# Optimization experiments

Measured on AMD Instinct MI355X. Metric: run time of the kernel, lower is better.

The kernel has to match this reference:

```python
import jax, jax.numpy as jnp
import numpy as np


def setup_inputs() -> dict:
    key = jax.random.key(0)
    k1, k2, k3, k4 = jax.random.split(key, 4)
    B, S, E, H = 8, 2048, 1024, 64
    x = jax.random.normal(k1, (B, S, E), dtype=jnp.float32)
    scale = 1.0 / np.sqrt(E)
    Wq = jax.random.normal(k2, (E, H), dtype=jnp.float32) * scale
    Wk = jax.random.normal(k3, (E, H), dtype=jnp.float32) * scale
    Wv = jax.random.normal(k4, (E, H), dtype=jnp.float32) * scale
    return {"x": x, "Wq": Wq, "Wk": Wk, "Wv": Wv}


def reference(x, Wq, Wk, Wv):
    # x: [B, S, E]; Wq/Wk/Wv: [E, H]
    B, S, E = x.shape
    H = Wq.shape[1]
    q = x @ Wq  # [B, S, H]
    k = x @ Wk
    v = x @ Wv
    inv_sqrt_h = 1.0 / jnp.sqrt(jnp.asarray(H, dtype=x.dtype))
    att = jnp.einsum("bqh,bkh->bqk", q, k) * inv_sqrt_h  # [B, S, S]
    causal = jnp.tril(jnp.ones((S, S), dtype=bool))
    att = jnp.where(causal, att, jnp.asarray(-jnp.inf, dtype=att.dtype))
    att = jax.nn.softmax(att, axis=-1)
    # dropout p=0.0 (eval) -> identity
    return jnp.einsum("bqk,bkh->bqh", att, v)  # [B, S, H]
```

## Files before the change

kernel.cpp:

```cpp
#include <hip/hip_runtime.h>
#include <math.h>

typedef __attribute__((ext_vector_type(8))) short bf16x8;
typedef __attribute__((ext_vector_type(16))) float fx16;

#define SEQ 2048
#define HD 64

__device__ __forceinline__ unsigned f2bf_bits(float f){
  unsigned u = __float_as_uint(f);
  return (u + 0x7fffu + ((u >> 16) & 1u)) >> 16;
}
__device__ __forceinline__ unsigned cvt_pk_bf16(float a, float b){
  unsigned r;
  asm("v_cvt_pk_bf16_f32 %0, %1, %2" : "=v"(r) : "v"(a), "v"(b));
  return r;
}
__device__ __forceinline__ float lo16f(unsigned u){ return __uint_as_float(u << 16); }
__device__ __forceinline__ float hi16f(unsigned u){ return __uint_as_float(u & 0xffff0000u); }
union U8 { bf16x8 v; short s[8]; unsigned u[4]; };

__device__ __forceinline__ fx16 mfma_bf16(bf16x8 a, bf16x8 b, fx16 c){
  return __builtin_amdgcn_mfma_f32_32x32x16_bf16(a, b, c, 0, 0, 0);
}
__device__ __forceinline__ fx16 fzero(){
  fx16 z;
#pragma unroll
  for (int i = 0; i < 16; ++i) z[i] = 0.f;
  return z;
}

__global__ __launch_bounds__(256) void wconv_kernel(
    const float* __restrict__ Wq, const float* __restrict__ Wk, const float* __restrict__ Wv,
    short* __restrict__ wsB)
{
  int gid = blockIdx.x * 4 + (threadIdx.x >> 6);
  int lane = threadIdx.x & 63;
  int l31 = lane & 31, h = lane >> 5;
  int half = gid & 1;
  int rem = gid >> 1;
  int t = rem % 6;
  int stage = rem / 6;
  int n = t * 32 + l31;
  int mat = n >> 6, col = n & 63;
  const float* W = (mat == 0) ? Wq : (mat == 1) ? Wk : Wv;
  int kbase = stage * 16 + h * 8;
  U8 o;
#pragma unroll
  for (int i = 0; i < 8; ++i) {
    float f = W[(size_t)(kbase + i) * 64 + col];
    unsigned hb = f2bf_bits(f);
    if (half == 0) o.s[i] = (short)hb;
    else {
      float hf = __uint_as_float(hb << 16);
      o.s[i] = (short)f2bf_bits(f - hf);
    }
  }
  *(bf16x8*)(wsB + (size_t)gid * 512 + lane * 8) = o.v;
}

__global__ __launch_bounds__(256) void proj_kernel(
    const float* __restrict__ x, const short* __restrict__ wsB,
    short* __restrict__ qh, short* __restrict__ ql,
    short* __restrict__ kh, short* __restrict__ kl,
    short* __restrict__ vth, short* __restrict__ vtl)
{
  __shared__ float Rx[6 * 16 * 64];
  __shared__ float Vb[32 * 68];

  const int tid = threadIdx.x;
  const int lane = tid & 63, w = tid >> 6;
  const int l31 = lane & 31, h = lane >> 5;
  const int nsel = w & 1;
  const int ksel = w >> 1;
  const int row0 = blockIdx.x * 32;
  const size_t xbase = (size_t)(row0 + l31) * 1024;

  fx16 acc[3];
#pragma unroll
  for (int t = 0; t < 3; ++t) acc[t] = fzero();

#pragma unroll 4
  for (int s = 0; s < 32; ++s) {
    const int stage = ksel * 32 + s;
    const int k = stage * 16 + h * 8;
    float4 fa = *(const float4*)(x + xbase + k);
    float4 fb = *(const float4*)(x + xbase + k + 4);
    U8 ah, al;
    ah.u[0] = cvt_pk_bf16(fa.x, fa.y);
    ah.u[1] = cvt_pk_bf16(fa.z, fa.w);
    ah.u[2] = cvt_pk_bf16(fb.x, fb.y);
    ah.u[3] = cvt_pk_bf16(fb.z, fb.w);
    al.u[0] = cvt_pk_bf16(fa.x - lo16f(ah.u[0]), fa.y - hi16f(ah.u[0]));
    al.u[1] = cvt_pk_bf16(fa.z - lo16f(ah.u[1]), fa.w - hi16f(ah.u[1]));
    al.u[2] = cvt_pk_bf16(fb.x - lo16f(ah.u[2]), fb.y - hi16f(ah.u[2]));
    al.u[3] = cvt_pk_bf16(fb.z - lo16f(ah.u[3]), fb.w - hi16f(ah.u[3]));
#pragma unroll
    for (int tt = 0; tt < 3; ++tt) {
      const int tg = nsel * 3 + tt;
      const size_t g2 = ((size_t)stage * 6 + tg) * 2;
      bf16x8 Bh = *(const bf16x8*)(wsB + g2 * 512 + lane * 8);
      bf16x8 Bl = *(const bf16x8*)(wsB + g2 * 512 + 512 + lane * 8);
      acc[tt] = mfma_bf16(al.v, Bh, acc[tt]);
      acc[tt] = mfma_bf16(ah.v, Bl, acc[tt]);
      acc[tt] = mfma_bf16(ah.v, Bh, acc[tt]);
    }
  }

  if (ksel == 1) {
#pragma unroll
    for (int t = 0; t < 3; ++t) {
      const int tg = nsel * 3 + t;
#pragma unroll
      for (int r = 0; r < 16; ++r)
        Rx[tg * 1024 + r * 64 + lane] = acc[t][r];
    }
  }
  __syncthreads();
  if (ksel == 0) {
#pragma unroll
    for (int t = 0; t < 3; ++t) {
      const int tg = nsel * 3 + t;
      const int mat = tg >> 1;
      const int colb = (tg & 1) * 32 + l31;
      if (mat < 2) {
        short* dh = (mat == 0) ? qh : kh;
        short* dl = (mat == 0) ? ql : kl;
#pragma unroll
        for (int r = 0; r < 16; ++r) {
          float f = acc[t][r] + Rx[tg * 1024 + r * 64 + lane];
          int rowg = row0 + (r & 3) + 8 * (r >> 2) + 4 * h;
          unsigned hb = f2bf_bits(f);
          float hf = __uint_as_float(hb << 16);
          unsigned lb = f2bf_bits(f - hf);
          dh[(size_t)rowg * 64 + colb] = (short)hb;
          dl[(size_t)rowg * 64 + colb] = (short)lb;
        }
      } else {
#pragma unroll
        for (int r = 0; r < 16; ++r) {
          float f = acc[t][r] + Rx[tg * 1024 + r * 64 + lane];
          int srel = (r & 3) + 8 * (r >> 2) + 4 * h;
          Vb[srel * 68 + (tg - 4) * 32 + l31] = f;
        }
      }
    }
  }
  __syncthreads();
  {
    int d = tid >> 2, s8 = (tid & 3) * 8;
    int bb = row0 >> 11, s0 = row0 & 2047;
    U8 hv, lv;
#pragma unroll
    for (int ss = 0; ss < 8; ++ss) {
      float f = Vb[(s8 + ss) * 68 + d];
      unsigned hb = f2bf_bits(f);
      float hf = __uint_as_float(hb << 16);
      hv.s[ss] = (short)hb;
      lv.s[ss] = (short)f2bf_bits(f - hf);
    }
    size_t o = (size_t)(bb * 64 + d) * 2048 + s0 + s8;
    *(bf16x8*)(vth + o) = hv.v;
    *(bf16x8*)(vtl + o) = lv.v;
  }
}

__global__ __launch_bounds__(64) void attn_kernel(
    const short* __restrict__ qh, const short* __restrict__ ql,
    const short* __restrict__ kh, const short* __restrict__ kl,
    const short* __restrict__ vth, const short* __restrict__ vtl,
    float* __restrict__ segO, float* __restrict__ segL, float* __restrict__ segM)
{
  const int bid = blockIdx.x;
  const int b = bid & 7;
  const int r = bid >> 3;
  int g = 0;
  while (r >= 4 * (g + 1) * (g + 2)) ++g;
  const int rr = r - 4 * g * (g + 1);
  const int qt = g * 8 + rr / (g + 1);
  const int sg = rr % (g + 1);
  const int nk = qt + 1;
  const int nsg = g + 1;
  const int bs = nk / nsg, rem = nk % nsg;
  const int nsteps = bs + (sg < rem ? 1 : 0);
  const int kt0 = sg * bs + (sg < rem ? sg : rem);

  const int lane = threadIdx.x;
  const int l31 = lane & 31, h = lane >> 5;
  const int qabs = qt * 32 + l31;

  bf16x8 qf0[4], qf1[4];
  {
    size_t qrow = ((size_t)b * 2048 + qabs) * 64;
#pragma unroll
    for (int ds = 0; ds < 4; ++ds) {
      qf0[ds] = *(const bf16x8*)(qh + qrow + ds * 16 + 8 * h);
      qf1[ds] = *(const bf16x8*)(ql + qrow + ds * 16 + 8 * h);
    }
  }

  fx16 acc0 = fzero(), acc1 = fzero();
  float Mrun = -3e38f, lrun = 0.f;

  bf16x8 kah[4], kal[4];
  {
    const size_t koff = ((size_t)b * 2048 + (size_t)kt0 * 32 + l31) * 64 + 8 * h;
#pragma unroll
    for (int ds = 0; ds < 4; ++ds) {
      kah[ds] = *(const bf16x8*)(kh + koff + ds * 16);
      kal[ds] = *(const bf16x8*)(kl + koff + ds * 16);
    }
  }

  for (int it = 0; it < nsteps; ++it) {
    const int kt = kt0 + it;
    bf16x8 vfh[2][2], vfl[2][2];
#pragma unroll
    for (int kp = 0; kp < 2; ++kp)
#pragma unroll
      for (int md = 0; md < 2; ++md) {
        const size_t vrow = (size_t)(b * 64 + md * 32 + l31) * 2048 + kt * 32 + kp * 16 + 8 * h;
        vfh[kp][md] = *(const bf16x8*)(vth + vrow);
        vfl[kp][md] = *(const bf16x8*)(vtl + vrow);
      }
    const int kn = (it + 1 < nsteps) ? kt + 1 : kt;
    bf16x8 knh[4], knl[4];
    {
      const size_t koff = ((size_t)b * 2048 + (size_t)kn * 32 + l31) * 64 + 8 * h;
#pragma unroll
      for (int ds = 0; ds < 4; ++ds) {
        knh[ds] = *(const bf16x8*)(kh + koff + ds * 16);
        knl[ds] = *(const bf16x8*)(kl + koff + ds * 16);
      }
    }

    fx16 stA = fzero(), stB = fzero();
    __builtin_amdgcn_s_setprio(1);
#pragma unroll
    for (int ds = 0; ds < 4; ++ds) {
      stA = mfma_bf16(kah[ds], qf0[ds], stA);
      stB = mfma_bf16(kal[ds], qf0[ds], stB);
      stB = mfma_bf16(kah[ds], qf1[ds], stB);
    }
    __builtin_amdgcn_s_setprio(0);

    float sv[16];
    const bool diag = (kt == qt);
#pragma unroll
    for (int r2 = 0; r2 < 16; ++r2) {
      float s = (stA[r2] + stB[r2]) * 0.125f;
      if (diag) {
        int ka = kt * 32 + (r2 & 3) + 8 * (r2 >> 2) + 4 * h;
        if (ka > qabs) s = -3e38f;
      }
      sv[r2] = s;
    }
    float tm = sv[0];
#pragma unroll
    for (int r2 = 1; r2 < 16; ++r2) tm = fmaxf(tm, sv[r2]);
    tm = fmaxf(tm, __shfl_xor(tm, 32, 64));
    float Mnew = fmaxf(Mrun, tm);
    float alpha = __expf(Mrun - Mnew);
    Mrun = Mnew;
    float psum = 0.f;
#pragma unroll
    for (int r2 = 0; r2 < 16; ++r2) { sv[r2] = __expf(sv[r2] - Mnew); psum += sv[r2]; }
    psum += __shfl_xor(psum, 32, 64);
    lrun = lrun * alpha + psum;
#pragma unroll
    for (int r2 = 0; r2 < 16; ++r2) { acc0[r2] *= alpha; acc1[r2] *= alpha; }

    unsigned chv[8], clv[8];
#pragma unroll
    for (int q2 = 0; q2 < 8; ++q2) {
      unsigned c = cvt_pk_bf16(sv[2 * q2], sv[2 * q2 + 1]);
      chv[q2] = c;
      clv[q2] = cvt_pk_bf16(sv[2 * q2] - lo16f(c), sv[2 * q2 + 1] - hi16f(c));
    }
#pragma unroll
    for (int kp = 0; kp < 2; ++kp) {
      U8 ph, pl;
      {
        unsigned c0 = chv[4 * kp], c1 = chv[4 * kp + 1], c2 = chv[4 * kp + 2], c3 = chv[4 * kp + 3];
        unsigned x0 = (unsigned)__shfl_xor((int)c0, 32, 64);
        unsigned x1 = (unsigned)__shfl_xor((int)c1, 32, 64);
        unsigned x2 = (unsigned)__shfl_xor((int)c2, 32, 64);
        unsigned x3 = (unsigned)__shfl_xor((int)c3, 32, 64);
        ph.u[0] = h ? x2 : c0;  ph.u[1] = h ? x3 : c1;
        ph.u[2] = h ? c2 : x0;  ph.u[3] = h ? c3 : x1;
        c0 = clv[4 * kp]; c1 = clv[4 * kp + 1]; c2 = clv[4 * kp + 2]; c3 = clv[4 * kp + 3];
        x0 = (unsigned)__shfl_xor((int)c0, 32, 64);
        x1 = (unsigned)__shfl_xor((int)c1, 32, 64);
        x2 = (unsigned)__shfl_xor((int)c2, 32, 64);
        x3 = (unsigned)__shfl_xor((int)c3, 32, 64);
        pl.u[0] = h ? x2 : c0;  pl.u[1] = h ? x3 : c1;
        pl.u[2] = h ? c2 : x0;  pl.u[3] = h ? c3 : x1;
      }
      __builtin_amdgcn_s_setprio(1);
      acc0 = mfma_bf16(vfl[kp][0], ph.v, acc0);
      acc0 = mfma_bf16(vfh[kp][0], pl.v, acc0);
      acc0 = mfma_bf16(vfh[kp][0], ph.v, acc0);
      acc1 = mfma_bf16(vfl[kp][1], ph.v, acc1);
      acc1 = mfma_bf16(vfh[kp][1], pl.v, acc1);
      acc1 = mfma_bf16(vfh[kp][1], ph.v, acc1);
      __builtin_amdgcn_s_setprio(0);
    }
#pragma unroll
    for (int ds = 0; ds < 4; ++ds) { kah[ds] = knh[ds]; kal[ds] = knl[ds]; }
  }

  float* o = segO + (size_t)bid * 2048;
#pragma unroll
  for (int md = 0; md < 2; ++md) {
#pragma unroll
    for (int r2 = 0; r2 < 16; ++r2) {
      int d = md * 32 + (r2 & 3) + 8 * (r2 >> 2) + 4 * h;
      float val = md ? acc1[r2] : acc0[r2];
      o[d * 32 + l31] = val;
    }
  }
  if (h == 0) {
    segL[(size_t)bid * 32 + l31] = lrun;
    segM[(size_t)bid * 32 + l31] = Mrun;
  }
}

__global__ __launch_bounds__(256) void combine_kernel(
    const float* __restrict__ segO, const float* __restrict__ segL,
    const float* __restrict__ segM, float* __restrict__ out)
{
  __shared__ float Sc[8][32];
  __shared__ float Linv[32];
  __shared__ float Ot[64 * 40];

  const int bq = blockIdx.x;
  const int b = bq >> 6, qt = bq & 63;
  const int g = qt >> 3, nsg = g + 1;
  const int base = 4 * g * (g + 1) + (qt & 7) * nsg;
  const int tid = threadIdx.x;

  if (tid < 32) {
    float M = -3e38f;
    for (int s = 0; s < nsg; ++s)
      M = fmaxf(M, segM[(size_t)((base + s) * 8 + b) * 32 + tid]);
    float L = 0.f;
    for (int s = 0; s < nsg; ++s) {
      float e = __expf(segM[(size_t)((base + s) * 8 + b) * 32 + tid] - M);
      Sc[s][tid] = e;
      L += e * segL[(size_t)((base + s) * 8 + b) * 32 + tid];
    }
    Linv[tid] = 1.f / L;
  }
  __syncthreads();
  {
#pragma unroll
    for (int i = tid; i < 512; i += 256) {
      int d = i >> 3, q4 = (i & 7) * 4;
      float4 acc = {0.f, 0.f, 0.f, 0.f};
      for (int s = 0; s < nsg; ++s) {
        float4 v = *(const float4*)(segO + (size_t)((base + s) * 8 + b) * 2048 + d * 32 + q4);
        acc.x += Sc[s][q4 + 0] * v.x;
        acc.y += Sc[s][q4 + 1] * v.y;
        acc.z += Sc[s][q4 + 2] * v.z;
        acc.w += Sc[s][q4 + 3] * v.w;
      }
      *(float4*)&Ot[d * 40 + q4] = acc;
    }
  }
  __syncthreads();
  {
    const int q = tid >> 3, dc = (tid & 7) * 8;
    const float inv = Linv[q];
    float* dst = out + ((size_t)b * 2048 + qt * 32 + q) * 64 + dc;
#pragma unroll
    for (int i = 0; i < 2; ++i) {
      float4 o;
      o.x = Ot[(dc + 4 * i + 0) * 40 + q] * inv;
      o.y = Ot[(dc + 4 * i + 1) * 40 + q] * inv;
      o.z = Ot[(dc + 4 * i + 2) * 40 + q] * inv;
      o.w = Ot[(dc + 4 * i + 3) * 40 + q] * inv;
      *(float4*)(dst + 4 * i) = o;
    }
  }
}

extern "C" void kernel_launch(void* const* d_in, const int* in_sizes, int n_in,
                              void* d_out, int out_size, void* d_ws, size_t ws_size,
                              hipStream_t stream) {
  const float* x  = (const float*)d_in[0];
  const float* Wq = (const float*)d_in[1];
  const float* Wk = (const float*)d_in[2];
  const float* Wv = (const float*)d_in[3];

  char* wsb = (char*)d_ws;
  short* wsB = (short*)(wsb + 0);
  short* qh  = (short*)(wsb + 786432);
  short* ql  = (short*)(wsb + 2883584);
  short* kh  = (short*)(wsb + 4980736);
  short* kl  = (short*)(wsb + 7077888);
  short* vth = (short*)(wsb + 9175040);
  short* vtl = (short*)(wsb + 11272192);
  float* segO = (float*)(wsb + 13369344);
  float* segL = (float*)(wsb + 32243712);
  float* segM = (float*)(wsb + 32538624);

  wconv_kernel<<<192, 256, 0, stream>>>(Wq, Wk, Wv, wsB);
  proj_kernel<<<512, 256, 0, stream>>>(x, wsB, qh, ql, kh, kl, vth, vtl);
  attn_kernel<<<2304, 64, 0, stream>>>(qh, ql, kh, kl, vth, vtl, segO, segL, segM);
  combine_kernel<<<512, 256, 0, stream>>>(segO, segL, segM, (float*)d_out);
}
```

Measured before the change: 97.79 us.

## Split projection K-reduction over 8 waves and use fixed 5-tile attention segments

The projection kernel now uses 512 threads, splitting the K dimension four ways instead of two, with a two-level shared-memory reduction of partial accumulators. The attention split-K scheme changes from group-based segments to fixed segments of at most five key tiles, which raises the block count to 3536 and evens out per-block work. The software prefetch of the next K tile is removed and K is loaded at the start of each step. The aim is more parallelism and better load balance, at the cost of extra reduction syncs, more segment partials for the combine kernel to read, and less latency hiding in attention.

```diff
diff --git a/kernel.cpp b/kernel.cpp
--- a/kernel.cpp
+++ b/kernel.cpp
@@ -59,20 +59,20 @@
   *(bf16x8*)(wsB + (size_t)gid * 512 + lane * 8) = o.v;
 }
 
-__global__ __launch_bounds__(256) void proj_kernel(
+__global__ __launch_bounds__(512) void proj_kernel(
     const float* __restrict__ x, const short* __restrict__ wsB,
     short* __restrict__ qh, short* __restrict__ ql,
     short* __restrict__ kh, short* __restrict__ kl,
     short* __restrict__ vth, short* __restrict__ vtl)
 {
-  __shared__ float Rx[6 * 16 * 64];
+  __shared__ float Rx[4][3 * 16 * 64];
   __shared__ float Vb[32 * 68];
 
   const int tid = threadIdx.x;
   const int lane = tid & 63, w = tid >> 6;
   const int l31 = lane & 31, h = lane >> 5;
+  const int ksel = w >> 1;
   const int nsel = w & 1;
-  const int ksel = w >> 1;
   const int row0 = blockIdx.x * 32;
   const size_t xbase = (size_t)(row0 + l31) * 1024;
 
@@ -81,8 +81,8 @@
   for (int t = 0; t < 3; ++t) acc[t] = fzero();
 
 #pragma unroll 4
-  for (int s = 0; s < 32; ++s) {
-    const int stage = ksel * 32 + s;
+  for (int s = 0; s < 16; ++s) {
+    const int stage = ksel * 16 + s;
     const int k = stage * 16 + h * 8;
     float4 fa = *(const float4*)(x + xbase + k);
     float4 fb = *(const float4*)(x + xbase + k + 4);
@@ -107,14 +107,30 @@
     }
   }
 
-  if (ksel == 1) {
-#pragma unroll
-    for (int t = 0; t < 3; ++t) {
-      const int tg = nsel * 3 + t;
+  if (ksel == 1 || ksel == 3) {
+    const int ws_ = (ksel == 1) ? nsel : 2 + nsel;
+#pragma unroll
+    for (int t = 0; t < 3; ++t)
 #pragma unroll
       for (int r = 0; r < 16; ++r)
-        Rx[tg * 1024 + r * 64 + lane] = acc[t][r];
-    }
+        Rx[ws_][t * 1024 + r * 64 + lane] = acc[t][r];
+  }
+  __syncthreads();
+  if (ksel == 0 || ksel == 2) {
+    const int rs_ = (ksel == 0) ? nsel : 2 + nsel;
+#pragma unroll
+    for (int t = 0; t < 3; ++t)
+#pragma unroll
+      for (int r = 0; r < 16; ++r)
+        acc[t][r] += Rx[rs_][t * 1024 + r * 64 + lane];
+  }
+  __syncthreads();
+  if (ksel == 2) {
+#pragma unroll
+    for (int t = 0; t < 3; ++t)
+#pragma unroll
+      for (int r = 0; r < 16; ++r)
+        Rx[nsel][t * 1024 + r * 64 + lane] = acc[t][r];
   }
   __syncthreads();
   if (ksel == 0) {
@@ -123,12 +139,15 @@
       const int tg = nsel * 3 + t;
       const int mat = tg >> 1;
       const int colb = (tg & 1) * 32 + l31;
+#pragma unroll
+      for (int r = 0; r < 16; ++r)
+        acc[t][r] += Rx[nsel][t * 1024 + r * 64 + lane];
       if (mat < 2) {
         short* dh = (mat == 0) ? qh : kh;
         short* dl = (mat == 0) ? ql : kl;
 #pragma unroll
         for (int r = 0; r < 16; ++r) {
-          float f = acc[t][r] + Rx[tg * 1024 + r * 64 + lane];
+          float f = acc[t][r];
           int rowg = row0 + (r & 3) + 8 * (r >> 2) + 4 * h;
           unsigned hb = f2bf_bits(f);
           float hf = __uint_as_float(hb << 16);
@@ -139,7 +158,7 @@
       } else {
 #pragma unroll
         for (int r = 0; r < 16; ++r) {
-          float f = acc[t][r] + Rx[tg * 1024 + r * 64 + lane];
+          float f = acc[t][r];
           int srel = (r & 3) + 8 * (r >> 2) + 4 * h;
           Vb[srel * 68 + (tg - 4) * 32 + l31] = f;
         }
@@ -147,7 +166,7 @@
     }
   }
   __syncthreads();
-  {
+  if (tid < 256) {
     int d = tid >> 2, s8 = (tid & 3) * 8;
     int bb = row0 >> 11, s0 = row0 & 2047;
     U8 hv, lv;
@@ -173,17 +192,13 @@
 {
   const int bid = blockIdx.x;
   const int b = bid & 7;
-  const int r = bid >> 3;
-  int g = 0;
-  while (r >= 4 * (g + 1) * (g + 2)) ++g;
-  const int rr = r - 4 * g * (g + 1);
-  const int qt = g * 8 + rr / (g + 1);
-  const int sg = rr % (g + 1);
+  int r = bid >> 3;
+  int qt = 0, acc = 0;
+  while (r >= acc + ((qt + 5) / 5)) { acc += (qt + 5) / 5; ++qt; }
+  const int sg = r - acc;
   const int nk = qt + 1;
-  const int nsg = g + 1;
-  const int bs = nk / nsg, rem = nk % nsg;
-  const int nsteps = bs + (sg < rem ? 1 : 0);
-  const int kt0 = sg * bs + (sg < rem ? sg : rem);
+  const int kt0 = sg * 5;
+  int nsteps = nk - kt0; if (nsteps > 5) nsteps = 5;
 
   const int lane = threadIdx.x;
   const int l31 = lane & 31, h = lane >> 5;
@@ -202,18 +217,17 @@
   fx16 acc0 = fzero(), acc1 = fzero();
   float Mrun = -3e38f, lrun = 0.f;
 
-  bf16x8 kah[4], kal[4];
-  {
-    const size_t koff = ((size_t)b * 2048 + (size_t)kt0 * 32 + l31) * 64 + 8 * h;
-#pragma unroll
-    for (int ds = 0; ds < 4; ++ds) {
-      kah[ds] = *(const bf16x8*)(kh + koff + ds * 16);
-      kal[ds] = *(const bf16x8*)(kl + koff + ds * 16);
-    }
-  }
-
   for (int it = 0; it < nsteps; ++it) {
     const int kt = kt0 + it;
+    bf16x8 kah[4], kal[4];
+    {
+      const size_t koff = ((size_t)b * 2048 + (size_t)kt * 32 + l31) * 64 + 8 * h;
+#pragma unroll
+      for (int ds = 0; ds < 4; ++ds) {
+        kah[ds] = *(const bf16x8*)(kh + koff + ds * 16);
+        kal[ds] = *(const bf16x8*)(kl + koff + ds * 16);
+      }
+    }
     bf16x8 vfh[2][2], vfl[2][2];
 #pragma unroll
     for (int kp = 0; kp < 2; ++kp)
@@ -223,16 +237,6 @@
         vfh[kp][md] = *(const bf16x8*)(vth + vrow);
         vfl[kp][md] = *(const bf16x8*)(vtl + vrow);
       }
-    const int kn = (it + 1 < nsteps) ? kt + 1 : kt;
-    bf16x8 knh[4], knl[4];
-    {
-      const size_t koff = ((size_t)b * 2048 + (size_t)kn * 32 + l31) * 64 + 8 * h;
-#pragma unroll
-      for (int ds = 0; ds < 4; ++ds) {
-        knh[ds] = *(const bf16x8*)(kh + koff + ds * 16);
-        knl[ds] = *(const bf16x8*)(kl + koff + ds * 16);
-      }
-    }
 
     fx16 stA = fzero(), stB = fzero();
     __builtin_amdgcn_s_setprio(1);
@@ -305,8 +309,6 @@
       acc1 = mfma_bf16(vfh[kp][1], ph.v, acc1);
       __builtin_amdgcn_s_setprio(0);
     }
-#pragma unroll
-    for (int ds = 0; ds < 4; ++ds) { kah[ds] = knh[ds]; kal[ds] = knl[ds]; }
   }
 
   float* o = segO + (size_t)bid * 2048;
@@ -329,14 +331,15 @@
     const float* __restrict__ segO, const float* __restrict__ segL,
     const float* __restrict__ segM, float* __restrict__ out)
 {
-  __shared__ float Sc[8][32];
+  __shared__ float Sc[13][32];
   __shared__ float Linv[32];
   __shared__ float Ot[64 * 40];
 
   const int bq = blockIdx.x;
   const int b = bq >> 6, qt = bq & 63;
-  const int g = qt >> 3, nsg = g + 1;
-  const int base = 4 * g * (g + 1) + (qt & 7) * nsg;
+  const int nsg = (qt + 5) / 5;
+  int base = 0;
+  for (int i = 0; i < qt; ++i) base += (i + 5) / 5;
   const int tid = threadIdx.x;
 
   if (tid < 32) {
@@ -356,15 +359,15 @@
 #pragma unroll
     for (int i = tid; i < 512; i += 256) {
       int d = i >> 3, q4 = (i & 7) * 4;
-      float4 acc = {0.f, 0.f, 0.f, 0.f};
+      float4 a = {0.f, 0.f, 0.f, 0.f};
       for (int s = 0; s < nsg; ++s) {
         float4 v = *(const float4*)(segO + (size_t)((base + s) * 8 + b) * 2048 + d * 32 + q4);
-        acc.x += Sc[s][q4 + 0] * v.x;
-        acc.y += Sc[s][q4 + 1] * v.y;
-        acc.z += Sc[s][q4 + 2] * v.z;
-        acc.w += Sc[s][q4 + 3] * v.w;
-      }
-      *(float4*)&Ot[d * 40 + q4] = acc;
+        a.x += Sc[s][q4 + 0] * v.x;
+        a.y += Sc[s][q4 + 1] * v.y;
+        a.z += Sc[s][q4 + 2] * v.z;
+        a.w += Sc[s][q4 + 3] * v.w;
+      }
+      *(float4*)&Ot[d * 40 + q4] = a;
     }
   }
   __syncthreads();
@@ -401,11 +404,11 @@
   short* vth = (short*)(wsb + 9175040);
   short* vtl = (short*)(wsb + 11272192);
   float* segO = (float*)(wsb + 13369344);
-  float* segL = (float*)(wsb + 32243712);
-  float* segM = (float*)(wsb + 32538624);
+  float* segL = (float*)(wsb + 42336256);
+  float* segM = (float*)(wsb + 42788864);
 
   wconv_kernel<<<192, 256, 0, stream>>>(Wq, Wk, Wv, wsB);
-  proj_kernel<<<512, 256, 0, stream>>>(x, wsB, qh, ql, kh, kl, vth, vtl);
-  attn_kernel<<<2304, 64, 0, stream>>>(qh, ql, kh, kl, vth, vtl, segO, segL, segM);
+  proj_kernel<<<512, 512, 0, stream>>>(x, wsB, qh, ql, kh, kl, vth, vtl);
+  attn_kernel<<<3536, 64, 0, stream>>>(qh, ql, kh, kl, vth, vtl, segO, segL, segM);
   combine_kernel<<<512, 256, 0, stream>>>(segO, segL, segM, (float*)d_out);
 }
```

Result: slower. 102.9 us (+5.3%).
